# Kernel optimization log

Hardware: AMD Instinct MI355X
Metric: run time of the kernel (lower is better)

Reference implementation:

```python
import jax, jax.numpy as jnp
import numpy as np
import math

HEADS = 4
DIM_HEAD = 32
EPS = 1e-5

def _ln_channels(x):
    # LayerNorm over channel axis (axis=1) of NCHW, no affine (eps=1e-5)
    mu = jnp.mean(x, axis=1, keepdims=True)
    var = jnp.mean((x - mu) ** 2, axis=1, keepdims=True)
    return (x - mu) * jax.lax.rsqrt(var + EPS)

def setup_inputs() -> dict:
    key = jax.random.key(0)
    k1, k2, k3, k4 = jax.random.split(key, 4)
    dim, inner = 256, HEADS * DIM_HEAD
    x = jax.random.normal(k1, (16, dim, 64, 64), dtype=jnp.float32)
    Wqkv = jax.random.normal(k2, (3 * inner, dim), dtype=jnp.float32) * (1.0 / math.sqrt(dim))
    Wout = jax.random.normal(k3, (dim, inner), dtype=jnp.float32) * (1.0 / math.sqrt(inner))
    bout = jax.random.normal(k4, (dim,), dtype=jnp.float32) * 0.01
    return {"x": x, "Wqkv": Wqkv, "Wout": Wout, "bout": bout}

def reference(x, Wqkv, Wout, bout):
    B, C, H, W = x.shape
    N = H * W
    inner = HEADS * DIM_HEAD
    # pre-norm (channel-wise LayerNorm via permute in torch)
    normed = _ln_channels(x)
    # 1x1 conv to qkv: [B, 3*inner, H, W]
    qkv = jnp.einsum('oc,bchw->bohw', Wqkv, normed)
    q, k, v = jnp.split(qkv, 3, axis=1)
    # [B, inner, H, W] -> [B, heads, N, dim_head]
    def to_heads(t):
        return t.reshape(B, HEADS, DIM_HEAD, N).transpose(0, 1, 3, 2)
    q, k, v = to_heads(q), to_heads(k), to_heads(v)
    q = jax.nn.softmax(q, axis=-1)          # over dim_head
    k = jax.nn.softmax(k, axis=-2)          # over N
    q = q / math.sqrt(DIM_HEAD)
    v = v / N
    context = jnp.einsum('bhnd,bhne->bhde', k, v)   # [B,h,d,d]
    out = jnp.einsum('bhde,bhnd->bhne', context, q) # [B,h,N,d]
    out = out.transpose(0, 1, 3, 2).reshape(B, inner, H, W)
    out = jnp.einsum('oc,bchw->bohw', Wout, out) + bout[None, :, None, None]
    out = _ln_channels(out)                  # LinearAttention.out_norm
    return out + x                           # residual
```

## Files before the change

kernel.cpp:

```cpp
#include <hip/hip_runtime.h>
#include <hip/hip_bf16.h>
#include <math.h>

#define BATCH 16
#define CH 256
#define NPOS 4096
#define INNER 128
#define HEADS 4
#define DH 32

typedef __hip_bfloat16 bf16;
typedef short bf8v __attribute__((ext_vector_type(8)));
typedef float f32x4 __attribute__((ext_vector_type(4)));

__device__ __forceinline__ float b2f(bf16 v) { return __bfloat162float(v); }
__device__ __forceinline__ float us2f(unsigned short u) {
    unsigned w = ((unsigned)u) << 16; float f; __builtin_memcpy(&f, &w, 4); return f;
}
__device__ __forceinline__ unsigned short f2us(float f) {
    bf16 h = __float2bfloat16(f); unsigned short u; __builtin_memcpy(&u, &h, 2); return u;
}
__device__ __forceinline__ bf16 f2b(float v) { return __float2bfloat16(v); }

__global__ __launch_bounds__(256)
void fused_qkv_kernel(const float* __restrict__ x, const float* __restrict__ Wqkv,
                      bf16* __restrict__ p, bf16* __restrict__ kvt) {
    __shared__ bf16 A[128 * 264];
    __shared__ bf16 Bb[128 * 32];
    __shared__ float stats[512];

    const int b = blockIdx.y, n0 = blockIdx.x * 128;
    const int tid = threadIdx.x;
    const int wave = tid >> 6, lane = tid & 63;
    const int wm = (wave >> 1) * 64, wn = (wave & 1) * 64;
    const int lrow = lane & 15, kq = lane >> 4;

    {
        const int n = tid & 127, chalf = tid >> 7;
        const float* xp = x + ((size_t)b * CH + chalf * 128) * NPOS + n0 + n;
        float s = 0.f, sq = 0.f;
        for (int i0 = 0; i0 < 128; i0 += 8) {
            bf8v bv;
            #pragma unroll
            for (int j = 0; j < 8; ++j) {
                float v = xp[(size_t)(i0 + j) * NPOS];
                s += v; sq += v * v;
                bv[j] = (short)f2us(v);
            }
            *(bf8v*)&A[n * 264 + chalf * 128 + i0] = bv;
        }
        stats[tid * 2] = s; stats[tid * 2 + 1] = sq;
    }
    __syncthreads();
    if (tid < 128) {
        float s  = stats[tid * 2] + stats[(tid + 128) * 2];
        float sq = stats[tid * 2 + 1] + stats[(tid + 128) * 2 + 1];
        float m = s * (1.f / 256.f);
        float var = sq * (1.f / 256.f) - m * m;
        stats[tid * 2] = m;
        stats[tid * 2 + 1] = rsqrtf(var + 1e-5f);
    }
    __syncthreads();
    {
        unsigned* A32 = (unsigned*)A;
        #pragma unroll 4
        for (int i = 0; i < 64; ++i) {
            int idx = i * 256 + tid;
            int c2 = idx & 127, n = idx >> 7;
            unsigned u = A32[n * 132 + c2];
            float m = stats[n * 2], rs = stats[n * 2 + 1];
            float v0 = (us2f((unsigned short)(u & 0xffffu)) - m) * rs;
            float v1 = (us2f((unsigned short)(u >> 16)) - m) * rs;
            A32[n * 132 + c2] = (unsigned)f2us(v0) | ((unsigned)f2us(v1) << 16);
        }
    }

    for (int ph = 0; ph < 3; ++ph) {
        const int colbase = (ph == 2) ? 0 : (ph + 1) * 128;
        f32x4 acc[4][4];
        #pragma unroll
        for (int i = 0; i < 4; ++i)
            #pragma unroll
            for (int j = 0; j < 4; ++j) acc[i][j] = (f32x4){0.f, 0.f, 0.f, 0.f};

        for (int k0 = 0; k0 < 256; k0 += 32) {
            __syncthreads();
            #pragma unroll
            for (int i = 0; i < 4; ++i) {
                int s = i * 256 + tid;
                int col = s >> 3, q4 = s & 7;
                float4 w = *(const float4*)&Wqkv[(size_t)(colbase + col) * 256 + k0 + q4 * 4];
                ushort4 wb;
                wb.x = f2us(w.x); wb.y = f2us(w.y); wb.z = f2us(w.z); wb.w = f2us(w.w);
                *(ushort4*)&Bb[col * 32 + q4 * 4] = wb;
            }
            __syncthreads();
            bf8v af[4], bfr[4];
            #pragma unroll
            for (int t = 0; t < 4; ++t)
                af[t] = *(const bf8v*)&A[(wm + t * 16 + lrow) * 264 + k0 + kq * 8];
            #pragma unroll
            for (int t = 0; t < 4; ++t)
                bfr[t] = *(const bf8v*)&Bb[(wn + t * 16 + lrow) * 32 + kq * 8];
            #pragma unroll
            for (int mt = 0; mt < 4; ++mt)
                #pragma unroll
                for (int nt = 0; nt < 4; ++nt)
                    acc[mt][nt] = __builtin_amdgcn_mfma_f32_16x16x32_bf16(
                        af[mt], bfr[nt], acc[mt][nt], 0, 0, 0);
        }

        if (ph < 2) {
            unsigned* B32 = (unsigned*)Bb;
            unsigned* kv32 = (unsigned*)kvt;
            for (int pr = 0; pr < 4; ++pr) {
                __syncthreads();
                if ((wave >> 1) == (pr >> 1)) {
                    int mtb = (pr & 1) * 2;
                    #pragma unroll
                    for (int mi = 0; mi < 2; ++mi) {
                        int mt = mtb + mi;
                        #pragma unroll
                        for (int nt = 0; nt < 4; ++nt)
                            #pragma unroll
                            for (int r = 0; r < 4; ++r) {
                                int rl = mi * 16 + kq * 4 + r;
                                Bb[rl * 128 + wn + nt * 16 + lrow] = f2b(acc[mt][nt][r]);
                            }
                    }
                }
                __syncthreads();
                #pragma unroll
                for (int i = 0; i < 8; ++i) {
                    int idx = i * 256 + tid;
                    int c2 = idx & 63, rl = idx >> 6;
                    kv32[(size_t)(b * NPOS + n0 + pr * 32 + rl) * 128 + ph * 64 + c2] =
                        B32[rl * 64 + c2];
                }
            }
        } else {
            __syncthreads();
            bf16* pt = A;
            #pragma unroll
            for (int mt = 0; mt < 4; ++mt)
                #pragma unroll
                for (int nt = 0; nt < 4; ++nt)
                    #pragma unroll
                    for (int r = 0; r < 4; ++r)
                        pt[(wm + mt * 16 + kq * 4 + r) * 132 + wn + nt * 16 + lrow] =
                            f2b(acc[mt][nt][r]);
            __syncthreads();
            {
                int row = tid >> 1, hp = (tid & 1) * 2;
                float s0 = 0.f, s1 = 0.f;
                #pragma unroll 8
                for (int j = 0; j < 32; ++j) s0 += __expf(b2f(pt[row * 132 + hp * 32 + j]));
                #pragma unroll 8
                for (int j = 0; j < 32; ++j) s1 += __expf(b2f(pt[row * 132 + hp * 32 + 32 + j]));
                stats[row * 4 + hp] = 1.f / s0;
                stats[row * 4 + hp + 1] = 1.f / s1;
            }
            __syncthreads();
            unsigned* pt32 = (unsigned*)pt;
            unsigned* pg32 = (unsigned*)p;
            #pragma unroll 4
            for (int i = 0; i < 32; ++i) {
                int idx = i * 256 + tid;
                int c2 = idx & 63, n = idx >> 6;
                unsigned u = pt32[n * 66 + c2];
                float rd = stats[n * 4 + (c2 >> 4)];
                float v0 = __expf(us2f((unsigned short)(u & 0xffffu))) * rd;
                float v1 = __expf(us2f((unsigned short)(u >> 16))) * rd;
                pg32[(size_t)(b * NPOS + n0 + n) * 64 + c2] =
                    (unsigned)f2us(v0) | ((unsigned)f2us(v1) << 16);
            }
        }
    }
}

__global__ __launch_bounds__(256)
void context_kernel(const bf16* __restrict__ kvt, float* __restrict__ ctxu,
                    float* __restrict__ separt) {
    __shared__ float ks[128][36];
    __shared__ float vs[128][36];
    __shared__ float red_se[4][32];
    int sp = blockIdx.x, h = blockIdx.y, b = blockIdx.z;
    int tid = threadIdx.x;
    int wave = tid >> 6, lane = tid & 63;
    int eg = lane & 7, dg = lane >> 3;
    int sd = tid & 31, sq = (tid >> 5) & 3;
    const int koff = h * DH, voff = 128 + h * DH;
    size_t rowbase = ((size_t)b * NPOS + sp * 1024) * 256;

    float acc[4][4] = {};
    float se_loc = 0.f;

    for (int nc = 0; nc < 1024; nc += 128) {
        for (int t = tid; t < 1024; t += 256) {
            int n = t >> 3, dq = t & 7;
            const bf16* row = kvt + rowbase + (size_t)(nc + n) * 256;
            ushort4 ku = *(const ushort4*)(row + koff + dq * 4);
            ushort4 vu = *(const ushort4*)(row + voff + dq * 4);
            f32x4 kf, vf;
            kf[0] = __expf(us2f(ku.x)); kf[1] = __expf(us2f(ku.y));
            kf[2] = __expf(us2f(ku.z)); kf[3] = __expf(us2f(ku.w));
            vf[0] = us2f(vu.x); vf[1] = us2f(vu.y); vf[2] = us2f(vu.z); vf[3] = us2f(vu.w);
            *(f32x4*)&ks[n][dq * 4] = kf;
            *(f32x4*)&vs[n][dq * 4] = vf;
        }
        __syncthreads();
        #pragma unroll 4
        for (int i = 0; i < 32; ++i) {
            int n = wave * 32 + i;
            f32x4 kv = *(const f32x4*)&ks[n][dg * 4];
            f32x4 vv = *(const f32x4*)&vs[n][eg * 4];
            #pragma unroll
            for (int j = 0; j < 4; ++j)
                #pragma unroll
                for (int i2 = 0; i2 < 4; ++i2)
                    acc[j][i2] += kv[j] * vv[i2];
        }
        if (tid < 128) {
            float s = 0.f;
            #pragma unroll 8
            for (int i = 0; i < 32; ++i) s += ks[sq * 32 + i][sd];
            se_loc += s;
        }
        __syncthreads();
    }

    if (tid < 128) red_se[sq][sd] = se_loc;
    float* red = &ks[0][0];
    #pragma unroll
    for (int j = 0; j < 4; ++j)
        #pragma unroll
        for (int i = 0; i < 4; ++i)
            red[(wave * 64 + lane) * 16 + j * 4 + i] = acc[j][i];
    __syncthreads();
    size_t bhsp = ((size_t)(b * HEADS + h) * 4 + sp);
    for (int idx = tid; idx < 1024; idx += 256) {
        int d = idx >> 5, e = idx & 31;
        int l = (d >> 2) * 8 + (e >> 2);
        int slot = (d & 3) * 4 + (e & 3);
        float s = 0.f;
        #pragma unroll
        for (int w = 0; w < 4; ++w) s += red[(w * 64 + l) * 16 + slot];
        ctxu[bhsp * 1024 + idx] = s;
    }
    if (tid < 32) {
        float s = red_se[0][tid] + red_se[1][tid] + red_se[2][tid] + red_se[3][tid];
        separt[bhsp * 32 + tid] = s;
    }
}

__global__ __launch_bounds__(256)
void wmod_kernel(const float* __restrict__ Wout, const float* __restrict__ ctxu,
                 const float* __restrict__ separt, bf16* __restrict__ wmod) {
    __shared__ float cs[4096];
    __shared__ float ses[128];
    int cg = blockIdx.x, b = blockIdx.y;
    int tid = threadIdx.x;
    for (int idx = tid; idx < 4096; idx += 256) {
        int hh = idx >> 10, rest = idx & 1023;
        float s = 0.f;
        #pragma unroll
        for (int sp = 0; sp < 4; ++sp)
            s += ctxu[(((size_t)(b * HEADS + hh) * 4) + sp) * 1024 + rest];
        cs[idx] = s;
    }
    if (tid < 128) {
        int hh = tid >> 5, d = tid & 31;
        float s = 0.f;
        #pragma unroll
        for (int sp = 0; sp < 4; ++sp)
            s += separt[(((size_t)(b * HEADS + hh) * 4) + sp) * 32 + d];
        ses[tid] = s;
    }
    __syncthreads();
    int c = cg * 32 + (tid & 31);
    int g = tid >> 5;
    int h = g >> 1, d0 = (g & 1) * 16;
    const float* wr = Wout + (size_t)c * INNER + h * DH;
    float w[32];
    #pragma unroll
    for (int i = 0; i < 8; ++i) {
        float4 t = *(const float4*)&wr[i * 4];
        w[i * 4] = t.x; w[i * 4 + 1] = t.y; w[i * 4 + 2] = t.z; w[i * 4 + 3] = t.w;
    }
    const float SCALE = 4.3158341e-05f;
    #pragma unroll
    for (int dd = 0; dd < 16; ++dd) {
        int d = d0 + dd;
        const float* cr = &cs[h * 1024 + d * 32];
        float s = 0.f;
        #pragma unroll
        for (int e4 = 0; e4 < 8; ++e4) {
            f32x4 t = *(const f32x4*)&cr[e4 * 4];
            s += w[e4 * 4] * t[0] + w[e4 * 4 + 1] * t[1]
               + w[e4 * 4 + 2] * t[2] + w[e4 * 4 + 3] * t[3];
        }
        float val = s * SCALE / ses[h * 32 + d];
        wmod[((size_t)b * CH + c) * INNER + h * DH + d] = f2b(val);
    }
}

__global__ __launch_bounds__(256)
void fused_out_kernel(const bf16* __restrict__ p, const bf16* __restrict__ wmod,
                      const float* __restrict__ bout, const float* __restrict__ x,
                      float* __restrict__ out) {
    __shared__ char lds[51200];
    bf16* Ap = (bf16*)lds;
    bf16* Bw = (bf16*)(lds + 34816);
    float* ct = (float*)lds;
    float* st = (float*)(lds + 34816);

    const int b = blockIdx.y, n0 = blockIdx.x * 128;
    const int tid = threadIdx.x;
    const int wave = tid >> 6, lane = tid & 63;
    const int wm = (wave >> 1) * 64, wn2 = (wave & 1) * 128;
    const int lrow = lane & 15, kq = lane >> 4;

    {
        const unsigned* pg32 = (const unsigned*)p;
        unsigned* A32 = (unsigned*)Ap;
        #pragma unroll 4
        for (int i = 0; i < 32; ++i) {
            int idx = i * 256 + tid;
            int c2 = idx & 63, n = idx >> 6;
            A32[n * 68 + c2] = pg32[(size_t)(b * NPOS + n0 + n) * 64 + c2];
        }
    }

    f32x4 acc[4][8];
    #pragma unroll
    for (int i = 0; i < 4; ++i)
        #pragma unroll
        for (int j = 0; j < 8; ++j) acc[i][j] = (f32x4){0.f, 0.f, 0.f, 0.f};

    const bf16* wb = wmod + (size_t)b * CH * INNER;
    for (int k0 = 0; k0 < 128; k0 += 32) {
        __syncthreads();
        #pragma unroll
        for (int i = 0; i < 4; ++i) {
            int s = i * 256 + tid;
            int col = s >> 2, q4 = s & 3;
            uint4 u = *(const uint4*)&wb[(size_t)col * 128 + k0 + q4 * 8];
            *(uint4*)&Bw[col * 32 + q4 * 8] = u;
        }
        __syncthreads();
        bf8v af[4], bfr[8];
        #pragma unroll
        for (int t = 0; t < 4; ++t)
            af[t] = *(const bf8v*)&Ap[(wm + t * 16 + lrow) * 136 + k0 + kq * 8];
        #pragma unroll
        for (int t = 0; t < 8; ++t)
            bfr[t] = *(const bf8v*)&Bw[(wn2 + t * 16 + lrow) * 32 + kq * 8];
        #pragma unroll
        for (int mt = 0; mt < 4; ++mt)
            #pragma unroll
            for (int nt = 0; nt < 8; ++nt)
                acc[mt][nt] = __builtin_amdgcn_mfma_f32_16x16x32_bf16(
                    af[mt], bfr[nt], acc[mt][nt], 0, 0, 0);
    }

    #pragma unroll
    for (int nt = 0; nt < 8; ++nt) {
        float bv = bout[wn2 + nt * 16 + lrow];
        #pragma unroll
        for (int mt = 0; mt < 4; ++mt)
            #pragma unroll
            for (int r = 0; r < 4; ++r) acc[mt][nt][r] += bv;
    }

    __syncthreads();
    #pragma unroll
    for (int mt = 0; mt < 4; ++mt)
        #pragma unroll
        for (int r = 0; r < 4; ++r) {
            float s = 0.f, sq = 0.f;
            #pragma unroll
            for (int nt = 0; nt < 8; ++nt) {
                float v = acc[mt][nt][r];
                s += v; sq += v * v;
            }
            #pragma unroll
            for (int m = 1; m <= 8; m <<= 1) {
                s += __shfl_xor(s, m, 64);
                sq += __shfl_xor(sq, m, 64);
            }
            if (lrow == 0) {
                int row = wm + mt * 16 + kq * 4 + r;
                st[(wave & 1) * 256 + row * 2] = s;
                st[(wave & 1) * 256 + row * 2 + 1] = sq;
            }
        }
    __syncthreads();
    if (tid < 128) {
        float s  = st[tid * 2] + st[256 + tid * 2];
        float sq = st[tid * 2 + 1] + st[256 + tid * 2 + 1];
        float m = s * (1.f / 256.f);
        float var = sq * (1.f / 256.f) - m * m;
        st[512 + tid * 2] = m;
        st[512 + tid * 2 + 1] = rsqrtf(var + 1e-5f);
    }
    __syncthreads();
    #pragma unroll
    for (int mt = 0; mt < 4; ++mt)
        #pragma unroll
        for (int r = 0; r < 4; ++r) {
            int row = wm + mt * 16 + kq * 4 + r;
            float m = st[512 + row * 2], rs = st[512 + row * 2 + 1];
            #pragma unroll
            for (int nt = 0; nt < 8; ++nt)
                acc[mt][nt][r] = (acc[mt][nt][r] - m) * rs;
        }

    for (int pr = 0; pr < 4; ++pr) {
        __syncthreads();
        if ((wave >> 1) == (pr >> 1)) {
            int mtb = (pr & 1) * 2;
            #pragma unroll
            for (int mi = 0; mi < 2; ++mi) {
                int mt = mtb + mi;
                #pragma unroll
                for (int nt = 0; nt < 8; ++nt)
                    #pragma unroll
                    for (int r = 0; r < 4; ++r) {
                        int rl = mi * 16 + kq * 4 + r;
                        ct[(wn2 + nt * 16 + lrow) * 33 + rl] = acc[mt][nt][r];
                    }
            }
        }
        __syncthreads();
        #pragma unroll 4
        for (int i = 0; i < 32; ++i) {
            int idx = i * 256 + tid;
            int n = idx & 31, c = idx >> 5;
            size_t gi = ((size_t)b * CH + c) * NPOS + n0 + pr * 32 + n;
            out[gi] = ct[c * 33 + n] + x[gi];
        }
    }
}

extern "C" void kernel_launch(void* const* d_in, const int* in_sizes, int n_in,
                              void* d_out, int out_size, void* d_ws, size_t ws_size,
                              hipStream_t stream) {
    const float* x    = (const float*)d_in[0];
    const float* Wqkv = (const float*)d_in[1];
    const float* Wout = (const float*)d_in[2];
    const float* bout = (const float*)d_in[3];
    float* out = (float*)d_out;

    char* ws = (char*)d_ws;
    bf16*  p      = (bf16*)ws;
    bf16*  kvt    = (bf16*)(ws + 16777216);
    float* ctxu   = (float*)(ws + 50331648);
    float* separt = (float*)(ws + 51380224);
    bf16*  wmod   = (bf16*)(ws + 51412992);

    fused_qkv_kernel<<<dim3(32, BATCH), 256, 0, stream>>>(x, Wqkv, p, kvt);
    context_kernel<<<dim3(4, HEADS, BATCH), 256, 0, stream>>>(kvt, ctxu, separt);
    wmod_kernel<<<dim3(8, BATCH), 256, 0, stream>>>(Wout, ctxu, separt, wmod);
    fused_out_kernel<<<dim3(32, BATCH), 256, 0, stream>>>(p, wmod, bout, x, out);
}
```

Before: 225.0 us.

## Pre-convert Wqkv to bf16, widen QKV kernel to 512 threads, fuse context+wmod

```diff
diff --git a/kernel.cpp b/kernel.cpp
--- a/kernel.cpp
+++ b/kernel.cpp
@@ -21,25 +21,39 @@
     bf16 h = __float2bfloat16(f); unsigned short u; __builtin_memcpy(&u, &h, 2); return u;
 }
 __device__ __forceinline__ bf16 f2b(float v) { return __float2bfloat16(v); }
+__device__ __forceinline__ void gload16(const void* g, void* l) {
+    __builtin_amdgcn_global_load_lds(
+        (__attribute__((address_space(1))) unsigned int*)(g),
+        (__attribute__((address_space(3))) unsigned int*)(l), 16, 0, 0);
+}
 
 __global__ __launch_bounds__(256)
-void fused_qkv_kernel(const float* __restrict__ x, const float* __restrict__ Wqkv,
+void convert_wq_kernel(const float* __restrict__ W, bf16* __restrict__ wq) {
+    int i = blockIdx.x * 256 + threadIdx.x;
+    float4 w = ((const float4*)W)[i];
+    ushort4 o;
+    o.x = f2us(w.x); o.y = f2us(w.y); o.z = f2us(w.z); o.w = f2us(w.w);
+    ((ushort4*)wq)[i] = o;
+}
+
+__global__ __launch_bounds__(512)
+void fused_qkv_kernel(const float* __restrict__ x, const bf16* __restrict__ wq,
                       bf16* __restrict__ p, bf16* __restrict__ kvt) {
     __shared__ bf16 A[128 * 264];
-    __shared__ bf16 Bb[128 * 32];
-    __shared__ float stats[512];
+    __shared__ bf16 Bb[32 * 132];
+    __shared__ float stats[1024];
 
     const int b = blockIdx.y, n0 = blockIdx.x * 128;
     const int tid = threadIdx.x;
     const int wave = tid >> 6, lane = tid & 63;
-    const int wm = (wave >> 1) * 64, wn = (wave & 1) * 64;
+    const int wm = (wave >> 2) * 64, wn = (wave & 3) * 32;
     const int lrow = lane & 15, kq = lane >> 4;
 
     {
-        const int n = tid & 127, chalf = tid >> 7;
-        const float* xp = x + ((size_t)b * CH + chalf * 128) * NPOS + n0 + n;
+        const int n = tid & 127, cq = tid >> 7;
+        const float* xp = x + ((size_t)b * CH + cq * 64) * NPOS + n0 + n;
         float s = 0.f, sq = 0.f;
-        for (int i0 = 0; i0 < 128; i0 += 8) {
+        for (int i0 = 0; i0 < 64; i0 += 8) {
             bf8v bv;
             #pragma unroll
             for (int j = 0; j < 8; ++j) {
@@ -47,14 +61,18 @@
                 s += v; sq += v * v;
                 bv[j] = (short)f2us(v);
             }
-            *(bf8v*)&A[n * 264 + chalf * 128 + i0] = bv;
+            *(bf8v*)&A[n * 264 + cq * 64 + i0] = bv;
         }
         stats[tid * 2] = s; stats[tid * 2 + 1] = sq;
     }
     __syncthreads();
     if (tid < 128) {
-        float s  = stats[tid * 2] + stats[(tid + 128) * 2];
-        float sq = stats[tid * 2 + 1] + stats[(tid + 128) * 2 + 1];
+        float s = 0.f, sq = 0.f;
+        #pragma unroll
+        for (int j = 0; j < 4; ++j) {
+            s  += stats[(tid + 128 * j) * 2];
+            sq += stats[(tid + 128 * j) * 2 + 1];
+        }
         float m = s * (1.f / 256.f);
         float var = sq * (1.f / 256.f) - m * m;
         stats[tid * 2] = m;
@@ -64,8 +82,8 @@
     {
         unsigned* A32 = (unsigned*)A;
         #pragma unroll 4
-        for (int i = 0; i < 64; ++i) {
-            int idx = i * 256 + tid;
+        for (int i = 0; i < 32; ++i) {
+            int idx = i * 512 + tid;
             int c2 = idx & 127, n = idx >> 7;
             unsigned u = A32[n * 132 + c2];
             float m = stats[n * 2], rs = stats[n * 2 + 1];
@@ -77,35 +95,28 @@
 
     for (int ph = 0; ph < 3; ++ph) {
         const int colbase = (ph == 2) ? 0 : (ph + 1) * 128;
-        f32x4 acc[4][4];
+        f32x4 acc[4][2];
         #pragma unroll
         for (int i = 0; i < 4; ++i)
             #pragma unroll
-            for (int j = 0; j < 4; ++j) acc[i][j] = (f32x4){0.f, 0.f, 0.f, 0.f};
-
+            for (int j = 0; j < 2; ++j) acc[i][j] = (f32x4){0.f, 0.f, 0.f, 0.f};
+
+        const int gcol = colbase + (tid >> 2), gq4 = tid & 3;
         for (int k0 = 0; k0 < 256; k0 += 32) {
             __syncthreads();
-            #pragma unroll
-            for (int i = 0; i < 4; ++i) {
-                int s = i * 256 + tid;
-                int col = s >> 3, q4 = s & 7;
-                float4 w = *(const float4*)&Wqkv[(size_t)(colbase + col) * 256 + k0 + q4 * 4];
-                ushort4 wb;
-                wb.x = f2us(w.x); wb.y = f2us(w.y); wb.z = f2us(w.z); wb.w = f2us(w.w);
-                *(ushort4*)&Bb[col * 32 + q4 * 4] = wb;
-            }
+            gload16(wq + (size_t)gcol * 256 + k0 + gq4 * 8, (char*)Bb + wave * 1024);
             __syncthreads();
-            bf8v af[4], bfr[4];
+            bf8v af[4], bfr[2];
             #pragma unroll
             for (int t = 0; t < 4; ++t)
                 af[t] = *(const bf8v*)&A[(wm + t * 16 + lrow) * 264 + k0 + kq * 8];
             #pragma unroll
-            for (int t = 0; t < 4; ++t)
+            for (int t = 0; t < 2; ++t)
                 bfr[t] = *(const bf8v*)&Bb[(wn + t * 16 + lrow) * 32 + kq * 8];
             #pragma unroll
             for (int mt = 0; mt < 4; ++mt)
                 #pragma unroll
-                for (int nt = 0; nt < 4; ++nt)
+                for (int nt = 0; nt < 2; ++nt)
                     acc[mt][nt] = __builtin_amdgcn_mfma_f32_16x16x32_bf16(
                         af[mt], bfr[nt], acc[mt][nt], 0, 0, 0);
         }
@@ -115,27 +126,27 @@
             unsigned* kv32 = (unsigned*)kvt;
             for (int pr = 0; pr < 4; ++pr) {
                 __syncthreads();
-                if ((wave >> 1) == (pr >> 1)) {
+                if ((wave >> 2) == (pr >> 1)) {
                     int mtb = (pr & 1) * 2;
                     #pragma unroll
                     for (int mi = 0; mi < 2; ++mi) {
                         int mt = mtb + mi;
                         #pragma unroll
-                        for (int nt = 0; nt < 4; ++nt)
+                        for (int nt = 0; nt < 2; ++nt)
                             #pragma unroll
                             for (int r = 0; r < 4; ++r) {
                                 int rl = mi * 16 + kq * 4 + r;
-                                Bb[rl * 128 + wn + nt * 16 + lrow] = f2b(acc[mt][nt][r]);
+                                Bb[rl * 132 + wn + nt * 16 + lrow] = f2b(acc[mt][nt][r]);
                             }
                     }
                 }
                 __syncthreads();
                 #pragma unroll
-                for (int i = 0; i < 8; ++i) {
-                    int idx = i * 256 + tid;
+                for (int i = 0; i < 4; ++i) {
+                    int idx = i * 512 + tid;
                     int c2 = idx & 63, rl = idx >> 6;
                     kv32[(size_t)(b * NPOS + n0 + pr * 32 + rl) * 128 + ph * 64 + c2] =
-                        B32[rl * 64 + c2];
+                        B32[rl * 66 + c2];
                 }
             }
         } else {
@@ -144,28 +155,25 @@
             #pragma unroll
             for (int mt = 0; mt < 4; ++mt)
                 #pragma unroll
-                for (int nt = 0; nt < 4; ++nt)
+                for (int nt = 0; nt < 2; ++nt)
                     #pragma unroll
                     for (int r = 0; r < 4; ++r)
                         pt[(wm + mt * 16 + kq * 4 + r) * 132 + wn + nt * 16 + lrow] =
                             f2b(acc[mt][nt][r]);
             __syncthreads();
             {
-                int row = tid >> 1, hp = (tid & 1) * 2;
-                float s0 = 0.f, s1 = 0.f;
+                int row = tid >> 2, h = tid & 3;
+                float s = 0.f;
                 #pragma unroll 8
-                for (int j = 0; j < 32; ++j) s0 += __expf(b2f(pt[row * 132 + hp * 32 + j]));
-                #pragma unroll 8
-                for (int j = 0; j < 32; ++j) s1 += __expf(b2f(pt[row * 132 + hp * 32 + 32 + j]));
-                stats[row * 4 + hp] = 1.f / s0;
-                stats[row * 4 + hp + 1] = 1.f / s1;
+                for (int j = 0; j < 32; ++j) s += __expf(b2f(pt[row * 132 + h * 32 + j]));
+                stats[row * 4 + h] = 1.f / s;
             }
             __syncthreads();
             unsigned* pt32 = (unsigned*)pt;
             unsigned* pg32 = (unsigned*)p;
             #pragma unroll 4
-            for (int i = 0; i < 32; ++i) {
-                int idx = i * 256 + tid;
+            for (int i = 0; i < 16; ++i) {
+                int idx = i * 512 + tid;
                 int c2 = idx & 63, n = idx >> 6;
                 unsigned u = pt32[n * 66 + c2];
                 float rd = stats[n * 4 + (c2 >> 4)];
@@ -178,25 +186,30 @@
     }
 }
 
-__global__ __launch_bounds__(256)
-void context_kernel(const bf16* __restrict__ kvt, float* __restrict__ ctxu,
-                    float* __restrict__ separt) {
-    __shared__ float ks[128][36];
-    __shared__ float vs[128][36];
-    __shared__ float red_se[4][32];
-    int sp = blockIdx.x, h = blockIdx.y, b = blockIdx.z;
-    int tid = threadIdx.x;
-    int wave = tid >> 6, lane = tid & 63;
-    int eg = lane & 7, dg = lane >> 3;
-    int sd = tid & 31, sq = (tid >> 5) & 3;
+__global__ __launch_bounds__(512)
+void context_wmod_kernel(const bf16* __restrict__ kvt, const float* __restrict__ Wout,
+                         bf16* __restrict__ wmod) {
+    __shared__ float kvbuf[2][128][36];
+    __shared__ float sep[4][32];
+    __shared__ float ses[32];
+    __shared__ float cs[1024];
+    float (*ks)[36] = kvbuf[0];
+    float (*vs)[36] = kvbuf[1];
+    float* red = &kvbuf[0][0][0];
+
+    const int h = blockIdx.x, b = blockIdx.y;
+    const int tid = threadIdx.x;
+    const int wave = tid >> 6, lane = tid & 63;
+    const int eg = lane & 7, dg = lane >> 3;
+    const int sd = tid & 31, sq = (tid >> 5) & 3;
     const int koff = h * DH, voff = 128 + h * DH;
-    size_t rowbase = ((size_t)b * NPOS + sp * 1024) * 256;
+    const size_t rowbase = (size_t)b * NPOS * 256;
 
     float acc[4][4] = {};
     float se_loc = 0.f;
 
-    for (int nc = 0; nc < 1024; nc += 128) {
-        for (int t = tid; t < 1024; t += 256) {
+    for (int nc = 0; nc < NPOS; nc += 128) {
+        for (int t = tid; t < 1024; t += 512) {
             int n = t >> 3, dq = t & 7;
             const bf16* row = kvt + rowbase + (size_t)(nc + n) * 256;
             ushort4 ku = *(const ushort4*)(row + koff + dq * 4);
@@ -210,8 +223,8 @@
         }
         __syncthreads();
         #pragma unroll 4
-        for (int i = 0; i < 32; ++i) {
-            int n = wave * 32 + i;
+        for (int i = 0; i < 16; ++i) {
+            int n = wave * 16 + i;
             f32x4 kv = *(const f32x4*)&ks[n][dg * 4];
             f32x4 vv = *(const f32x4*)&vs[n][eg * 4];
             #pragma unroll
@@ -229,57 +242,27 @@
         __syncthreads();
     }
 
-    if (tid < 128) red_se[sq][sd] = se_loc;
-    float* red = &ks[0][0];
+    if (tid < 128) sep[sq][sd] = se_loc;
+    __syncthreads();
     #pragma unroll
     for (int j = 0; j < 4; ++j)
         #pragma unroll
         for (int i = 0; i < 4; ++i)
             red[(wave * 64 + lane) * 16 + j * 4 + i] = acc[j][i];
     __syncthreads();
-    size_t bhsp = ((size_t)(b * HEADS + h) * 4 + sp);
-    for (int idx = tid; idx < 1024; idx += 256) {
-        int d = idx >> 5, e = idx & 31;
+    if (tid < 32) ses[tid] = sep[0][tid] + sep[1][tid] + sep[2][tid] + sep[3][tid];
+    for (int t = tid; t < 1024; t += 512) {
+        int d = t >> 5, e = t & 31;
         int l = (d >> 2) * 8 + (e >> 2);
         int slot = (d & 3) * 4 + (e & 3);
         float s = 0.f;
         #pragma unroll
-        for (int w = 0; w < 4; ++w) s += red[(w * 64 + l) * 16 + slot];
-        ctxu[bhsp * 1024 + idx] = s;
-    }
-    if (tid < 32) {
-        float s = red_se[0][tid] + red_se[1][tid] + red_se[2][tid] + red_se[3][tid];
-        separt[bhsp * 32 + tid] = s;
-    }
-}
-
-__global__ __launch_bounds__(256)
-void wmod_kernel(const float* __restrict__ Wout, const float* __restrict__ ctxu,
-                 const float* __restrict__ separt, bf16* __restrict__ wmod) {
-    __shared__ float cs[4096];
-    __shared__ float ses[128];
-    int cg = blockIdx.x, b = blockIdx.y;
-    int tid = threadIdx.x;
-    for (int idx = tid; idx < 4096; idx += 256) {
-        int hh = idx >> 10, rest = idx & 1023;
-        float s = 0.f;
-        #pragma unroll
-        for (int sp = 0; sp < 4; ++sp)
-            s += ctxu[(((size_t)(b * HEADS + hh) * 4) + sp) * 1024 + rest];
-        cs[idx] = s;
-    }
-    if (tid < 128) {
-        int hh = tid >> 5, d = tid & 31;
-        float s = 0.f;
-        #pragma unroll
-        for (int sp = 0; sp < 4; ++sp)
-            s += separt[(((size_t)(b * HEADS + hh) * 4) + sp) * 32 + d];
-        ses[tid] = s;
-    }
-    __syncthreads();
-    int c = cg * 32 + (tid & 31);
-    int g = tid >> 5;
-    int h = g >> 1, d0 = (g & 1) * 16;
+        for (int w = 0; w < 8; ++w) s += red[(w * 64 + l) * 16 + slot];
+        cs[t] = s;
+    }
+    __syncthreads();
+
+    const int c = tid >> 1, d0 = (tid & 1) * 16;
     const float* wr = Wout + (size_t)c * INNER + h * DH;
     float w[32];
     #pragma unroll
@@ -288,10 +271,11 @@
         w[i * 4] = t.x; w[i * 4 + 1] = t.y; w[i * 4 + 2] = t.z; w[i * 4 + 3] = t.w;
     }
     const float SCALE = 4.3158341e-05f;
+    float val[16];
     #pragma unroll
     for (int dd = 0; dd < 16; ++dd) {
         int d = d0 + dd;
-        const float* cr = &cs[h * 1024 + d * 32];
+        const float* cr = &cs[d * 32];
         float s = 0.f;
         #pragma unroll
         for (int e4 = 0; e4 < 8; ++e4) {
@@ -299,9 +283,13 @@
             s += w[e4 * 4] * t[0] + w[e4 * 4 + 1] * t[1]
                + w[e4 * 4 + 2] * t[2] + w[e4 * 4 + 3] * t[3];
         }
-        float val = s * SCALE / ses[h * 32 + d];
-        wmod[((size_t)b * CH + c) * INNER + h * DH + d] = f2b(val);
-    }
+        val[dd] = s * SCALE / ses[d];
+    }
+    unsigned* wm32 = (unsigned*)wmod;
+    size_t base = (size_t)(b * CH + c) * 64 + h * 16 + (d0 >> 1);
+    #pragma unroll
+    for (int i = 0; i < 8; ++i)
+        wm32[base + i] = (unsigned)f2us(val[2 * i]) | ((unsigned)f2us(val[2 * i + 1]) << 16);
 }
 
 __global__ __launch_bounds__(256)
@@ -452,14 +440,13 @@
     float* out = (float*)d_out;
 
     char* ws = (char*)d_ws;
-    bf16*  p      = (bf16*)ws;
-    bf16*  kvt    = (bf16*)(ws + 16777216);
-    float* ctxu   = (float*)(ws + 50331648);
-    float* separt = (float*)(ws + 51380224);
-    bf16*  wmod   = (bf16*)(ws + 51412992);
-
-    fused_qkv_kernel<<<dim3(32, BATCH), 256, 0, stream>>>(x, Wqkv, p, kvt);
-    context_kernel<<<dim3(4, HEADS, BATCH), 256, 0, stream>>>(kvt, ctxu, separt);
-    wmod_kernel<<<dim3(8, BATCH), 256, 0, stream>>>(Wout, ctxu, separt, wmod);
+    bf16* p    = (bf16*)ws;
+    bf16* kvt  = (bf16*)(ws + 16777216);
+    bf16* wmod = (bf16*)(ws + 50331648);
+    bf16* wq   = (bf16*)(ws + 51380224);
+
+    convert_wq_kernel<<<96, 256, 0, stream>>>(Wqkv, wq);
+    fused_qkv_kernel<<<dim3(32, BATCH), 512, 0, stream>>>(x, wq, p, kvt);
+    context_wmod_kernel<<<dim3(HEADS, BATCH), 512, 0, stream>>>(kvt, Wout, wmod);
     fused_out_kernel<<<dim3(32, BATCH), 256, 0, stream>>>(p, wmod, bout, x, out);
 }
```

Result: slower. 234.6 us (+4.3%).
